# Kernel tuning notes

Hardware: AMD Instinct MI355X
Metric: run time of the kernel (lower is better)

## Reference

```python
import jax, jax.numpy as jnp
import numpy as np

NUM_SCALE_LAYERS = [16, 8, 8]


def _pool2s1(x):
    # MaxPool1d(kernel=2, stride=1): length L -> L-1
    return jnp.maximum(x[..., :-1], x[..., 1:])


def _pool3s2(x):
    # MaxPool1d(kernel=3, stride=2): length L -> (L-3)//2 + 1
    L = x.shape[-1]
    n = (L - 3) // 2 + 1
    return jnp.maximum(jnp.maximum(x[..., 0:2 * n:2], x[..., 1:2 * n + 1:2]),
                       x[..., 2:2 * n + 2:2])


def setup_inputs() -> dict:
    key = jax.random.key(0)
    x = jax.random.normal(key, (32, 512, 64), dtype=jnp.float32)
    return {"x": x}


def reference(x):
    B, H, N = x.shape
    ori = N  # scale 0 has stride-1 first layer, so ori_num_clips == N
    map_h = jnp.zeros((B, H, ori, ori), dtype=x.dtype)
    map_mask = jnp.zeros((B, 1, ori, ori), dtype=x.dtype)
    acum = 0
    stride = 1
    for scale_idx, num_layer in enumerate(NUM_SCALE_LAYERS):
        for i in range(num_layer):
            if i == 0:
                if scale_idx > 0:
                    x = _pool3s2(x)
                    stride *= 2
                # scale 0 first layer is MaxPool1d(1,1) == identity, stride*=1
            else:
                x = _pool2s1(x)
            # diagonal scatter directly into the original-resolution map
            s_idx = np.arange(0, ori - acum - i * stride, stride)
            e_idx = s_idx + acum + i * stride
            map_h = map_h.at[:, :, s_idx, e_idx].set(x)
            map_mask = map_mask.at[:, :, s_idx, e_idx].set(jnp.ones((), x.dtype))
        acum += stride * (num_layer + 1)
    return map_h, map_mask
```

## Files before the change

### kernel.cpp

```cpp
#include <hip/hip_runtime.h>


#define BB 32
#define HH 512
#define NN 64

typedef float f32x4 __attribute__((ext_vector_type(4)));

__device__ __forceinline__ unsigned long long active_mask_for_e(int e) {
    unsigned long long m;
    if (e >= 15) m = 0xFFFFull << (e - 15);
    else         m = 0xFFFFull >> (15 - e);
    if ((e & 1) && e >= 17) {
        int a = e - 31; if (a < 0) a = 0;
        int b = e - 17;
        unsigned long long r = (~0ull >> (63 - b)) & (~0ull << a);
        m |= r & 0x5555555555555555ull;
    }
    if (((e & 3) == 3) && e >= 35) {
        int b = e - 35;
        unsigned long long r = (~0ull >> (63 - b));
        m |= r & 0x1111111111111111ull;
    }
    return m;
}

__global__ __launch_bounds__(256) void sppool_fused_kernel(
        const float* __restrict__ x, float* __restrict__ map_h,
        float* __restrict__ map_mask) {
    __shared__ float sp[16][7][68];

    const int tid  = threadIdx.x;
    const int lrow = tid >> 4;
    const int lcol = tid & 15;
    const size_t rowbase = (size_t)blockIdx.x * 16;

    const float* xin = x + rowbase * NN;
    const f32x4 xv = ((const f32x4*)xin)[tid];
    *(f32x4*)&sp[lrow][0][lcol << 2] = xv;
    __syncthreads();

    #pragma unroll
    for (int k = 1; k <= 6; ++k) {
        const int off = 1 << (k - 1);
        float v[4];
        #pragma unroll
        for (int ii = 0; ii < 4; ++ii) {
            const int i = lcol + ii * 16;
            int p = i + off; if (p > 63) p = 63;
            v[ii] = fmaxf(sp[lrow][k - 1][i], sp[lrow][k - 1][p]);
        }
        __syncthreads();
        #pragma unroll
        for (int ii = 0; ii < 4; ++ii)
            sp[lrow][k][lcol + ii * 16] = v[ii];
        __syncthreads();
    }

    const int wave = tid >> 6;
    const int lane = tid & 63;
    const int sg   = lane >> 4;
    const int e0   = (lane & 15) << 2;

    const unsigned long long am0 = active_mask_for_e(e0 + 0);
    const unsigned long long am1 = active_mask_for_e(e0 + 1);
    const unsigned long long am2 = active_mask_for_e(e0 + 2);
    const unsigned long long am3 = active_mask_for_e(e0 + 3);

    #pragma unroll
    for (int rr = 0; rr < 4; ++rr) {
        const int lr = rr * 4 + wave;
        const float* rowsp = &sp[lr][0][0];
        float* outr = map_h + (rowbase + lr) * (size_t)(NN * NN) + e0;

        #pragma unroll 4
        for (int t = 0; t < 16; ++t) {
            const int s = (t << 2) + sg;
            f32x4 v;
            #pragma unroll
            for (int j = 0; j < 4; ++j) {
                const int e = e0 + j;
                int n = e - s + 1; if (n < 1) n = 1;
                const int k = 31 - __clz(n);
                const float lo = rowsp[k * 68 + s];
                const float hi = rowsp[k * 68 + (e + 1 - (1 << k))];
                const unsigned long long am = (j == 0) ? am0 : (j == 1) ? am1
                                            : (j == 2) ? am2 : am3;
                v[j] = ((am >> s) & 1ull) ? fmaxf(lo, hi) : 0.0f;
            }
            __builtin_nontemporal_store(
                v, reinterpret_cast<f32x4*>(outr + (size_t)s * NN));
        }
    }

    if (blockIdx.x < BB) {
        f32x4* mout = reinterpret_cast<f32x4*>(
            map_mask + (size_t)blockIdx.x * (NN * NN));
        #pragma unroll
        for (int kk = 0; kk < 4; ++kk) {
            const int idx = kk * 256 + tid;
            const int eg  = (idx & 15) << 2;
            const int s   = idx >> 4;
            f32x4 v;
            v.x = ((active_mask_for_e(eg + 0) >> s) & 1ull) ? 1.0f : 0.0f;
            v.y = ((active_mask_for_e(eg + 1) >> s) & 1ull) ? 1.0f : 0.0f;
            v.z = ((active_mask_for_e(eg + 2) >> s) & 1ull) ? 1.0f : 0.0f;
            v.w = ((active_mask_for_e(eg + 3) >> s) & 1ull) ? 1.0f : 0.0f;
            __builtin_nontemporal_store(v, mout + idx);
        }
    }
}

extern "C" void kernel_launch(void* const* d_in, const int* in_sizes, int n_in,
                              void* d_out, int out_size, void* d_ws, size_t ws_size,
                              hipStream_t stream) {
    const float* x = (const float*)d_in[0];
    float* map_h    = (float*)d_out;
    float* map_mask = (float*)d_out + (size_t)BB * HH * NN * NN;

    sppool_fused_kernel<<<BB * HH / 16, 256, 0, stream>>>(x, map_h, map_mask);
}
```

Before: 267.9 us.

## Assign one row per wave with shuffle-based pooling and regular stores

Each block now handles 4 rows, one per wave, instead of 16. The sparse-table max pyramid is built with wave shuffles and a wave barrier in place of block-wide __syncthreads, which also shrinks shared memory to raise occupancy (launch bounds now request 8 blocks). Nontemporal stores to the large output map are replaced by ordinary stores. The grid becomes four times larger and each block does less work, which may add launch and scheduling overhead. Dropping the nontemporal hint may also change cache behaviour for the write-bound output.

```diff
diff --git a/kernel.cpp b/kernel.cpp
--- a/kernel.cpp
+++ b/kernel.cpp
@@ -25,72 +25,54 @@
     return m;
 }
 
-__global__ __launch_bounds__(256) void sppool_fused_kernel(
+__global__ __launch_bounds__(256, 8) void sppool_fused_kernel(
         const float* __restrict__ x, float* __restrict__ map_h,
         float* __restrict__ map_mask) {
-    __shared__ float sp[16][7][68];
+    __shared__ float sp[4][7][68];
 
     const int tid  = threadIdx.x;
-    const int lrow = tid >> 4;
-    const int lcol = tid & 15;
-    const size_t rowbase = (size_t)blockIdx.x * 16;
+    const int wv   = tid >> 6;
+    const int lane = tid & 63;
+    const int row  = blockIdx.x * 4 + wv;
 
-    const float* xin = x + rowbase * NN;
-    const f32x4 xv = ((const f32x4*)xin)[tid];
-    *(f32x4*)&sp[lrow][0][lcol << 2] = xv;
-    __syncthreads();
-
+    float v = x[(size_t)row * NN + lane];
+    sp[wv][0][lane] = v;
     #pragma unroll
     for (int k = 1; k <= 6; ++k) {
-        const int off = 1 << (k - 1);
-        float v[4];
-        #pragma unroll
-        for (int ii = 0; ii < 4; ++ii) {
-            const int i = lcol + ii * 16;
-            int p = i + off; if (p > 63) p = 63;
-            v[ii] = fmaxf(sp[lrow][k - 1][i], sp[lrow][k - 1][p]);
-        }
-        __syncthreads();
-        #pragma unroll
-        for (int ii = 0; ii < 4; ++ii)
-            sp[lrow][k][lcol + ii * 16] = v[ii];
-        __syncthreads();
+        int p = lane + (1 << (k - 1)); if (p > 63) p = 63;
+        const float o = __shfl(v, p);
+        v = fmaxf(v, o);
+        sp[wv][k][lane] = v;
     }
+    __builtin_amdgcn_wave_barrier();
 
-    const int wave = tid >> 6;
-    const int lane = tid & 63;
-    const int sg   = lane >> 4;
-    const int e0   = (lane & 15) << 2;
+    const int sg = lane >> 4;
+    const int e0 = (lane & 15) << 2;
 
     const unsigned long long am0 = active_mask_for_e(e0 + 0);
     const unsigned long long am1 = active_mask_for_e(e0 + 1);
     const unsigned long long am2 = active_mask_for_e(e0 + 2);
     const unsigned long long am3 = active_mask_for_e(e0 + 3);
 
-    #pragma unroll
-    for (int rr = 0; rr < 4; ++rr) {
-        const int lr = rr * 4 + wave;
-        const float* rowsp = &sp[lr][0][0];
-        float* outr = map_h + (rowbase + lr) * (size_t)(NN * NN) + e0;
+    const float* rowsp = &sp[wv][0][0];
+    float* outr = map_h + (size_t)row * (NN * NN) + e0;
 
-        #pragma unroll 4
-        for (int t = 0; t < 16; ++t) {
-            const int s = (t << 2) + sg;
-            f32x4 v;
-            #pragma unroll
-            for (int j = 0; j < 4; ++j) {
-                const int e = e0 + j;
-                int n = e - s + 1; if (n < 1) n = 1;
-                const int k = 31 - __clz(n);
-                const float lo = rowsp[k * 68 + s];
-                const float hi = rowsp[k * 68 + (e + 1 - (1 << k))];
-                const unsigned long long am = (j == 0) ? am0 : (j == 1) ? am1
-                                            : (j == 2) ? am2 : am3;
-                v[j] = ((am >> s) & 1ull) ? fmaxf(lo, hi) : 0.0f;
-            }
-            __builtin_nontemporal_store(
-                v, reinterpret_cast<f32x4*>(outr + (size_t)s * NN));
+    #pragma unroll 4
+    for (int t = 0; t < 16; ++t) {
+        const int s = (t << 2) + sg;
+        f32x4 o;
+        #pragma unroll
+        for (int j = 0; j < 4; ++j) {
+            const int e = e0 + j;
+            int n = e - s + 1; if (n < 1) n = 1;
+            const int k = 31 - __clz(n);
+            const float lo = rowsp[k * 68 + s];
+            const float hi = rowsp[k * 68 + (e + 1 - (1 << k))];
+            const unsigned long long am = (j == 0) ? am0 : (j == 1) ? am1
+                                        : (j == 2) ? am2 : am3;
+            o[j] = ((am >> s) & 1ull) ? fmaxf(lo, hi) : 0.0f;
         }
+        *reinterpret_cast<f32x4*>(outr + (size_t)s * NN) = o;
     }
 
     if (blockIdx.x < BB) {
@@ -101,12 +83,12 @@
             const int idx = kk * 256 + tid;
             const int eg  = (idx & 15) << 2;
             const int s   = idx >> 4;
-            f32x4 v;
-            v.x = ((active_mask_for_e(eg + 0) >> s) & 1ull) ? 1.0f : 0.0f;
-            v.y = ((active_mask_for_e(eg + 1) >> s) & 1ull) ? 1.0f : 0.0f;
-            v.z = ((active_mask_for_e(eg + 2) >> s) & 1ull) ? 1.0f : 0.0f;
-            v.w = ((active_mask_for_e(eg + 3) >> s) & 1ull) ? 1.0f : 0.0f;
-            __builtin_nontemporal_store(v, mout + idx);
+            f32x4 mv;
+            mv.x = ((active_mask_for_e(eg + 0) >> s) & 1ull) ? 1.0f : 0.0f;
+            mv.y = ((active_mask_for_e(eg + 1) >> s) & 1ull) ? 1.0f : 0.0f;
+            mv.z = ((active_mask_for_e(eg + 2) >> s) & 1ull) ? 1.0f : 0.0f;
+            mv.w = ((active_mask_for_e(eg + 3) >> s) & 1ull) ? 1.0f : 0.0f;
+            mout[idx] = mv;
         }
     }
 }
@@ -118,5 +100,5 @@
     float* map_h    = (float*)d_out;
     float* map_mask = (float*)d_out + (size_t)BB * HH * NN * NN;
 
-    sppool_fused_kernel<<<BB * HH / 16, 256, 0, stream>>>(x, map_h, map_mask);
+    sppool_fused_kernel<<<BB * HH / 4, 256, 0, stream>>>(x, map_h, map_mask);
 }
```

Result: faster. 258.0 us (median of 2 runs) (-3.7%).
